# Kernel optimization log

Measured on AMD Instinct MI355X. Metric: run time of the kernel, lower is better.

Reference implementation:

```python
import jax, jax.numpy as jnp
import numpy as np

CODEBOOK_SIZE = 8192
EMBED_DIM = 256


def setup_inputs() -> dict:
    key = jax.random.key(0)
    k1, k2 = jax.random.split(key)
    z = jax.random.normal(k1, (8, 4096, EMBED_DIM), dtype=jnp.float32)
    # matches torch init: uniform_(-1/codebook_size, 1/codebook_size)
    codebook = jax.random.uniform(
        k2, (CODEBOOK_SIZE, EMBED_DIM), dtype=jnp.float32,
        minval=-1.0 / CODEBOOK_SIZE, maxval=1.0 / CODEBOOK_SIZE)
    return {"z": z, "codebook": codebook}


def reference(z, codebook):
    # z: [B, S, D]; codebook: [K, D]
    z_flat = z.reshape(-1, z.shape[-1])                      # [N, D]
    # ||z||^2 - 2 z.E^T + ||E||^2  -> [N, K]
    distances = (
        jnp.sum(z_flat * z_flat, axis=1, keepdims=True)
        - 2.0 * jnp.einsum("nd,kd->nk", z_flat, codebook)
        + jnp.sum(codebook * codebook, axis=1)
    )
    encoding_indices = jnp.argmin(distances, axis=1)         # [N]
    z_q = codebook[encoding_indices].reshape(z.shape)        # [B, S, D]
    return z_q, encoding_indices
```

## Files before the change

### kernel.cpp

```cpp
#include <hip/hip_runtime.h>


#define NROWS 32768
#define DIM   256
#define KCB   8192
#define CANDCAP 128
#define MARGIN  4.5e-4f
#define WBUF    320
#define NTILE   512

#define OFF_CAND  0
#define OFF_CNT   2097152
#define OFF_ZSQ   2129920
#define OFF_CSQ   2162688
#define OFF_CSQ1  2170880
#define OFF_OVL   2179072
#define OFF_OVC   2211840
#define OFF_IMG   2211856
#define OFF_IDX   8388608

using bf16x8 = __attribute__((ext_vector_type(8))) short;
using f32x4  = __attribute__((ext_vector_type(4))) float;

__device__ __forceinline__ unsigned short bf16rne(float f) {
    unsigned u = __float_as_uint(f);
    unsigned r = u + 0x7FFFu + ((u >> 16) & 1u);
    return (unsigned short)(r >> 16);
}

__device__ float np_sumsq_256(const float* __restrict__ p) {
#pragma clang fp contract(off)
    float blk[2];
    #pragma unroll
    for (int b = 0; b < 2; ++b) {
        const float* q = p + b * 128;
        float r[8];
        #pragma unroll
        for (int j = 0; j < 8; ++j) r[j] = __fmul_rn(q[j], q[j]);
        for (int i = 8; i < 128; i += 8) {
            #pragma unroll
            for (int j = 0; j < 8; ++j)
                r[j] = __fadd_rn(r[j], __fmul_rn(q[i + j], q[i + j]));
        }
        blk[b] = __fadd_rn(
            __fadd_rn(__fadd_rn(r[0], r[1]), __fadd_rn(r[2], r[3])),
            __fadd_rn(__fadd_rn(r[4], r[5]), __fadd_rn(r[6], r[7])));
    }
    return __fadd_rn(blk[0], blk[1]);
}

__global__ void vq_sumsq2_kernel(const float* __restrict__ z,
                                 const float* __restrict__ cb,
                                 float* __restrict__ zsq, float* __restrict__ csq) {
    int r = blockIdx.x * 256 + threadIdx.x;
    if (r < NROWS) zsq[r] = np_sumsq_256(z + (size_t)r * DIM);
    else if (r < NROWS + KCB) csq[r - NROWS] = np_sumsq_256(cb + (size_t)(r - NROWS) * DIM);
}

__global__ void vq_prepB_kernel(const float* __restrict__ cb,
                                const float* __restrict__ csq,
                                char* __restrict__ img, float* __restrict__ csq1,
                                unsigned* __restrict__ cnt, unsigned* __restrict__ ovc) {
    int t = blockIdx.x * 256 + threadIdx.x;
    if (t < NROWS) cnt[t] = 0;
    if (t == 0) *ovc = 0;
    if (t < 262144) {
        int s = t & 63, kk = (t >> 6) & 7, T = t >> 9;
        int code = s & 15, lhi = s >> 4;
        const float* src = cb + (size_t)(T * 16 + code) * DIM + kk * 32 + lhi * 8;
        float4 v0 = *reinterpret_cast<const float4*>(src);
        float4 v1 = *reinterpret_cast<const float4*>(src + 4);
        uint4 o;
        o.x = (unsigned)bf16rne(v0.x) | ((unsigned)bf16rne(v0.y) << 16);
        o.y = (unsigned)bf16rne(v0.z) | ((unsigned)bf16rne(v0.w) << 16);
        o.z = (unsigned)bf16rne(v1.x) | ((unsigned)bf16rne(v1.y) << 16);
        o.w = (unsigned)bf16rne(v1.z) | ((unsigned)bf16rne(v1.w) << 16);
        *reinterpret_cast<uint4*>(img + (size_t)T * 8192 + kk * 1024 + s * 16) = o;
    } else if (t < 262144 + KCB) {
        csq1[t - 262144] = csq[t - 262144] + 1.0f;
    }
}

__global__ __launch_bounds__(512, 2) void vq_screen_kernel(
    const float* __restrict__ z, const char* __restrict__ img,
    const float* __restrict__ csq1,
    unsigned* __restrict__ cnt, unsigned short* __restrict__ cand) {
    __shared__ unsigned runmin[128];
    __shared__ unsigned wcnt[8];
    __shared__ unsigned wbuf[8][WBUF];
    const int tid = threadIdx.x, lane = tid & 63, wid = tid >> 6;
    const int wr = wid >> 2, wc = wid & 3;
    const int l15 = lane & 15, lhi = lane >> 4;
    const int row0 = blockIdx.x * 128;
    const int tbase = wc * 128;

    bf16x8 ah[4][8];
    #pragma unroll
    for (int m = 0; m < 4; ++m) {
        const float* zr = z + (size_t)(row0 + wr * 64 + m * 16 + l15) * DIM;
        #pragma unroll
        for (int kk = 0; kk < 8; ++kk) {
            float4 v0 = *reinterpret_cast<const float4*>(zr + kk * 32 + lhi * 8);
            float4 v1 = *reinterpret_cast<const float4*>(zr + kk * 32 + lhi * 8 + 4);
            uint4 o;
            o.x = (unsigned)bf16rne(v0.x) | ((unsigned)bf16rne(v0.y) << 16);
            o.y = (unsigned)bf16rne(v0.z) | ((unsigned)bf16rne(v0.w) << 16);
            o.z = (unsigned)bf16rne(v1.x) | ((unsigned)bf16rne(v1.y) << 16);
            o.w = (unsigned)bf16rne(v1.z) | ((unsigned)bf16rne(v1.w) << 16);
            ah[m][kk] = __builtin_bit_cast(bf16x8, o);
        }
    }

    if (tid < 128) runmin[tid] = 0x7F800000u;
    if (tid < 8) wcnt[tid] = 0;
    __syncthreads();

    f32x4 acc[4];
    #pragma unroll
    for (int m = 0; m < 4; ++m) acc[m] = (f32x4){0.f, 0.f, 0.f, 0.f};

    const char*  gp = img + (size_t)tbase * 8192 + (size_t)lane * 16;
    const float* cp = csq1 + tbase * 16 + l15;
    int codeb = tbase * 16 + l15;

    uint4 bA[8]; float csA;
    uint4 bB[8]; float csB;

    auto PUSH = [&](int lr, int code) {
        unsigned pi = atomicAdd(&wcnt[wid], 1u);
        if (pi < WBUF) wbuf[wid][pi] = ((unsigned)lr << 13) | (unsigned)code;
        else {
            int grow = row0 + lr;
            unsigned gs = atomicAdd(&cnt[grow], 1u);
            if (gs < CANDCAP) cand[(size_t)grow * CANDCAP + gs] = (unsigned short)code;
        }
    };

#define LOADR(bh, cs)                                                     \
    {                                                                     \
        _Pragma("unroll")                                                 \
        for (int kk = 0; kk < 8; ++kk)                                    \
            bh[kk] = *reinterpret_cast<const uint4*>(gp + kk * 1024);     \
        cs = *cp;                                                         \
        gp += 8192; cp += 16;                                             \
    }

#define MFMAS(bh)                                                         \
    {                                                                     \
        __builtin_amdgcn_s_setprio(1);                                    \
        _Pragma("unroll")                                                 \
        for (int kk = 0; kk < 8; ++kk) {                                  \
            bf16x8 bhv = __builtin_bit_cast(bf16x8, bh[kk]);              \
            _Pragma("unroll")                                             \
            for (int m = 0; m < 4; ++m)                                   \
                acc[m] = __builtin_amdgcn_mfma_f32_16x16x32_bf16(         \
                    ah[m][kk], bhv, acc[m], 0, 0, 0);                     \
        }                                                                 \
        __builtin_amdgcn_s_setprio(0);                                    \
    }

#define EPI(csv)                                                          \
    {                                                                     \
        _Pragma("unroll")                                                 \
        for (int m = 0; m < 4; ++m) {                                     \
            const int lr0 = wr * 64 + m * 16 + lhi * 4;                   \
            uint4 rmb = *reinterpret_cast<const uint4*>(&runmin[lr0]);    \
            float s0 = fmaf(acc[m][0], -2.0f, csv);                       \
            float s1 = fmaf(acc[m][1], -2.0f, csv);                       \
            float s2 = fmaf(acc[m][2], -2.0f, csv);                       \
            float s3 = fmaf(acc[m][3], -2.0f, csv);                       \
            bool c0 = s0 < __uint_as_float(rmb.x) + MARGIN;               \
            bool c1 = s1 < __uint_as_float(rmb.y) + MARGIN;               \
            bool c2 = s2 < __uint_as_float(rmb.z) + MARGIN;               \
            bool c3 = s3 < __uint_as_float(rmb.w) + MARGIN;               \
            if (__any(c0 | c1 | c2 | c3)) {                               \
                if (c0) { if (s0 < __uint_as_float(rmb.x)) atomicMin(&runmin[lr0 + 0], __float_as_uint(s0)); PUSH(lr0 + 0, codeb); } \
                if (c1) { if (s1 < __uint_as_float(rmb.y)) atomicMin(&runmin[lr0 + 1], __float_as_uint(s1)); PUSH(lr0 + 1, codeb); } \
                if (c2) { if (s2 < __uint_as_float(rmb.z)) atomicMin(&runmin[lr0 + 2], __float_as_uint(s2)); PUSH(lr0 + 2, codeb); } \
                if (c3) { if (s3 < __uint_as_float(rmb.w)) atomicMin(&runmin[lr0 + 3], __float_as_uint(s3)); PUSH(lr0 + 3, codeb); } \
            }                                                             \
            acc[m] = (f32x4){0.f, 0.f, 0.f, 0.f};                         \
        }                                                                 \
        codeb += 16;                                                      \
    }

    LOADR(bA, csA);
    LOADR(bB, csB);
    MFMAS(bA);
    {
        #pragma unroll
        for (int m = 0; m < 4; ++m) {
            const int lr0 = wr * 64 + m * 16 + lhi * 4;
            #pragma unroll
            for (int r = 0; r < 4; ++r) {
                float s2 = fmaf(acc[m][r], -2.0f, csA);
                float sm = s2;
                sm = fminf(sm, __shfl_xor(sm, 1));
                sm = fminf(sm, __shfl_xor(sm, 2));
                sm = fminf(sm, __shfl_xor(sm, 4));
                sm = fminf(sm, __shfl_xor(sm, 8));
                if (l15 == 0) atomicMin(&runmin[lr0 + r], __float_as_uint(sm));
                if (s2 < sm + MARGIN) PUSH(lr0 + r, codeb);
            }
            acc[m] = (f32x4){0.f, 0.f, 0.f, 0.f};
        }
        codeb += 16;
    }
    LOADR(bA, csA);
    MFMAS(bB);
    EPI(csB);

    for (int ct = 2; ct < 128; ct += 2) {
        LOADR(bB, csB);
        MFMAS(bA);
        EPI(csA);
        LOADR(bA, csA);
        MFMAS(bB);
        EPI(csB);
    }

    unsigned n = wcnt[wid]; if (n > WBUF) n = WBUF;
    for (unsigned e = lane; e < n; e += 64) {
        unsigned u = wbuf[wid][e];
        int row = row0 + (int)(u >> 13);
        int code = (int)(u & 8191u);
        unsigned slot = atomicAdd(&cnt[row], 1u);
        if (slot < CANDCAP) cand[(size_t)row * CANDCAP + slot] = (unsigned short)code;
    }
#undef LOADR
#undef MFMAS
#undef EPI
}

__global__ __launch_bounds__(256) void vq_exact_kernel(
    const float* __restrict__ z, const float* __restrict__ cb,
    const float* __restrict__ zsq, const float* __restrict__ csq,
    const unsigned* __restrict__ cnt, const unsigned short* __restrict__ cand,
    unsigned* __restrict__ ovl, unsigned* __restrict__ ovc,
    float* __restrict__ idxF) {
    __shared__ float zrow[4][DIM];
    const int wid = threadIdx.x >> 6, lane = threadIdx.x & 63;
    const int row = blockIdx.x * 4 + wid;

    float4 zv4 = *reinterpret_cast<const float4*>(&z[(size_t)row * DIM + lane * 4]);
    *reinterpret_cast<float4*>(&zrow[wid][lane * 4]) = zv4;
    __syncthreads();

    const unsigned c = cnt[row];
    if (c == 0 || c > CANDCAP) {
        if (lane == 0) { unsigned s = atomicAdd(ovc, 1u); ovl[s] = row; }
        return;
    }

    const float Zr = zsq[row];
    const float4* cb4 = reinterpret_cast<const float4*>(cb);
    float best = 3.4e38f;
    int   bi   = 0x7FFFFFFF;

    for (int j = lane; j < (int)c; j += 64) {
        int k = cand[(size_t)row * CANDCAP + j];
        float a = 0.0f;
        #pragma unroll 8
        for (int q = 0; q < 64; ++q) {
            float4 cv = cb4[(size_t)k * 64 + q];
            float4 zv = *reinterpret_cast<const float4*>(&zrow[wid][q * 4]);
            a = fmaf(zv.x, cv.x, a); a = fmaf(zv.y, cv.y, a);
            a = fmaf(zv.z, cv.z, a); a = fmaf(zv.w, cv.w, a);
        }
        float sv = __fadd_rn(__fsub_rn(Zr, __fmul_rn(2.0f, a)), csq[k]);
        if (sv < best || (sv == best && k < bi)) { best = sv; bi = k; }
    }
    #pragma unroll
    for (int mk = 32; mk >= 1; mk >>= 1) {
        float ov = __shfl_xor(best, mk);
        int   oi = __shfl_xor(bi, mk);
        if (ov < best || (ov == best && oi < bi)) { best = ov; bi = oi; }
    }
    if (lane == 0) idxF[row] = (float)bi;
}

__global__ __launch_bounds__(256) void vq_cleanup_kernel(
    const float* __restrict__ z, const float* __restrict__ cb,
    const float* __restrict__ zsq, const float* __restrict__ csq,
    const unsigned* __restrict__ ovl, const unsigned* __restrict__ ovc,
    float* __restrict__ idxF) {
    __shared__ float zrow[DIM];
    __shared__ float wv[4]; __shared__ int wi[4];
    const int lane = threadIdx.x & 63, wid = threadIdx.x >> 6;
    const unsigned count = *ovc;
    for (unsigned w = blockIdx.x; w < count; w += gridDim.x) {
        const int row = ovl[w];
        __syncthreads();
        *reinterpret_cast<float4*>(&zrow[threadIdx.x * 4 & (DIM - 1)]) =
            *reinterpret_cast<const float4*>(&z[(size_t)row * DIM + (threadIdx.x * 4 & (DIM - 1))]);
        __syncthreads();
        const float Zr = zsq[row];
        const float4* cb4 = reinterpret_cast<const float4*>(cb);
        float best = 3.4e38f; int bi = 0x7FFFFFFF;
        for (int k = threadIdx.x; k < KCB; k += 256) {
            float a = 0.0f;
            #pragma unroll 8
            for (int q = 0; q < 64; ++q) {
                float4 cv = cb4[(size_t)k * 64 + q];
                float4 zv = *reinterpret_cast<const float4*>(&zrow[q * 4]);
                a = fmaf(zv.x, cv.x, a); a = fmaf(zv.y, cv.y, a);
                a = fmaf(zv.z, cv.z, a); a = fmaf(zv.w, cv.w, a);
            }
            float sv = __fadd_rn(__fsub_rn(Zr, __fmul_rn(2.0f, a)), csq[k]);
            if (sv < best || (sv == best && k < bi)) { best = sv; bi = k; }
        }
        #pragma unroll
        for (int mk = 32; mk >= 1; mk >>= 1) {
            float ov = __shfl_xor(best, mk);
            int   oi = __shfl_xor(bi, mk);
            if (ov < best || (ov == best && oi < bi)) { best = ov; bi = oi; }
        }
        if (lane == 0) { wv[wid] = best; wi[wid] = bi; }
        __syncthreads();
        if (threadIdx.x == 0) {
            #pragma unroll
            for (int u = 1; u < 4; ++u)
                if (wv[u] < best || (wv[u] == best && wi[u] < bi)) { best = wv[u]; bi = wi[u]; }
            idxF[row] = (float)bi;
        }
    }
}

__global__ void vq_gather_kernel(const float* __restrict__ cb,
                                 const float* __restrict__ idxF,
                                 float4* __restrict__ out4) {
    int g = blockIdx.x * blockDim.x + threadIdx.x;
    const float4* cb4 = reinterpret_cast<const float4*>(cb);
    for (int i = g; i < NROWS * 64; i += gridDim.x * blockDim.x) {
        int row = i >> 6, q = i & 63;
        int idx = (int)idxF[row];
        out4[i] = cb4[(size_t)idx * 64 + q];
    }
}

extern "C" void kernel_launch(void* const* d_in, const int* in_sizes, int n_in,
                              void* d_out, int out_size, void* d_ws, size_t ws_size,
                              hipStream_t stream) {
    const float* z  = (const float*)d_in[0];
    const float* cb = (const float*)d_in[1];
    float* out = (float*)d_out;

    unsigned short* candp = (unsigned short*)(out + OFF_CAND);
    unsigned*       cntp  = (unsigned*)(out + OFF_CNT);
    float*          zsq   = out + OFF_ZSQ;
    float*          csq   = out + OFF_CSQ;
    float*          csq1  = out + OFF_CSQ1;
    unsigned*       ovl   = (unsigned*)(out + OFF_OVL);
    unsigned*       ovc   = (unsigned*)(out + OFF_OVC);
    char*           img   = (char*)(out + OFF_IMG);
    float*          idxF  = out + OFF_IDX;

    vq_sumsq2_kernel<<<(NROWS + KCB) / 256, 256, 0, stream>>>(z, cb, zsq, csq);
    vq_prepB_kernel<<<1057, 256, 0, stream>>>(cb, csq, img, csq1, cntp, ovc);
    vq_screen_kernel<<<NROWS / 128, 512, 0, stream>>>(z, img, csq1, cntp, candp);
    vq_exact_kernel<<<NROWS / 4, 256, 0, stream>>>(z, cb, zsq, csq, cntp, candp, ovl, ovc, idxF);
    vq_cleanup_kernel<<<64, 256, 0, stream>>>(z, cb, zsq, csq, ovl, ovc, idxF);
    vq_gather_kernel<<<2048, 256, 0, stream>>>(cb, idxF, (float4*)out);
}
```

Before: 299.0 us.

## Merge prep kernels, fuse gather into exact/cleanup using workspace scratch

Folds the sum-of-squares kernel into the codebook bf16 packing kernel so one launch computes both norms and the image. When the workspace is large enough, scratch buffers move from the output to the workspace, so the exact and cleanup kernels can write the gathered codebook rows directly and the separate gather kernel is skipped. Also drops the MFMA priority hints in the screen kernel. This removes two launches and one pass over the indices, but adds a workspace-size dependency and an extra sync in cleanup.

Result: faster. 288.2 us (-3.6%).

```diff
diff --git a/kernel.cpp b/kernel.cpp
--- a/kernel.cpp
+++ b/kernel.cpp
@@ -7,17 +7,16 @@
 #define CANDCAP 128
 #define MARGIN  4.5e-4f
 #define WBUF    320
-#define NTILE   512
-
-#define OFF_CAND  0
-#define OFF_CNT   2097152
-#define OFF_ZSQ   2129920
-#define OFF_CSQ   2162688
-#define OFF_CSQ1  2170880
-#define OFF_OVL   2179072
-#define OFF_OVC   2211840
-#define OFF_IMG   2211856
-#define OFF_IDX   8388608
+
+#define SB_CAND  0u
+#define SB_CNT   8388608u
+#define SB_ZSQ   8519680u
+#define SB_CSQ   8650752u
+#define SB_CSQ1  8683520u
+#define SB_OVL   8716288u
+#define SB_OVC   8847360u
+#define SB_IMG   8847424u
+#define SB_NEED  13049920u
 
 using bf16x8 = __attribute__((ext_vector_type(8))) short;
 using f32x4  = __attribute__((ext_vector_type(4))) float;
@@ -49,18 +48,12 @@
     return __fadd_rn(blk[0], blk[1]);
 }
 
-__global__ void vq_sumsq2_kernel(const float* __restrict__ z,
-                                 const float* __restrict__ cb,
-                                 float* __restrict__ zsq, float* __restrict__ csq) {
-    int r = blockIdx.x * 256 + threadIdx.x;
-    if (r < NROWS) zsq[r] = np_sumsq_256(z + (size_t)r * DIM);
-    else if (r < NROWS + KCB) csq[r - NROWS] = np_sumsq_256(cb + (size_t)(r - NROWS) * DIM);
-}
-
-__global__ void vq_prepB_kernel(const float* __restrict__ cb,
-                                const float* __restrict__ csq,
-                                char* __restrict__ img, float* __restrict__ csq1,
-                                unsigned* __restrict__ cnt, unsigned* __restrict__ ovc) {
+__global__ void vq_prep_kernel(const float* __restrict__ z,
+                               const float* __restrict__ cb,
+                               char* __restrict__ img,
+                               float* __restrict__ zsq, float* __restrict__ csq,
+                               float* __restrict__ csq1,
+                               unsigned* __restrict__ cnt, unsigned* __restrict__ ovc) {
     int t = blockIdx.x * 256 + threadIdx.x;
     if (t < NROWS) cnt[t] = 0;
     if (t == 0) *ovc = 0;
@@ -77,7 +70,13 @@
         o.w = (unsigned)bf16rne(v1.z) | ((unsigned)bf16rne(v1.w) << 16);
         *reinterpret_cast<uint4*>(img + (size_t)T * 8192 + kk * 1024 + s * 16) = o;
     } else if (t < 262144 + KCB) {
-        csq1[t - 262144] = csq[t - 262144] + 1.0f;
+        int k = t - 262144;
+        float s = np_sumsq_256(cb + (size_t)k * DIM);
+        csq[k] = s;
+        csq1[k] = s + 1.0f;
+    } else if (t < 262144 + KCB + NROWS) {
+        int r = t - 262144 - KCB;
+        zsq[r] = np_sumsq_256(z + (size_t)r * DIM);
     }
 }
 
@@ -147,7 +146,6 @@
 
 #define MFMAS(bh)                                                         \
     {                                                                     \
-        __builtin_amdgcn_s_setprio(1);                                    \
         _Pragma("unroll")                                                 \
         for (int kk = 0; kk < 8; ++kk) {                                  \
             bf16x8 bhv = __builtin_bit_cast(bf16x8, bh[kk]);              \
@@ -156,7 +154,6 @@
                 acc[m] = __builtin_amdgcn_mfma_f32_16x16x32_bf16(         \
                     ah[m][kk], bhv, acc[m], 0, 0, 0);                     \
         }                                                                 \
-        __builtin_amdgcn_s_setprio(0);                                    \
     }
 
 #define EPI(csv)                                                          \
@@ -237,7 +234,7 @@
     const float* __restrict__ zsq, const float* __restrict__ csq,
     const unsigned* __restrict__ cnt, const unsigned short* __restrict__ cand,
     unsigned* __restrict__ ovl, unsigned* __restrict__ ovc,
-    float* __restrict__ idxF) {
+    float* __restrict__ idxF, float4* __restrict__ outz, int fused) {
     __shared__ float zrow[4][DIM];
     const int wid = threadIdx.x >> 6, lane = threadIdx.x & 63;
     const int row = blockIdx.x * 4 + wid;
@@ -277,15 +274,17 @@
         if (ov < best || (ov == best && oi < bi)) { best = ov; bi = oi; }
     }
     if (lane == 0) idxF[row] = (float)bi;
+    if (fused) outz[(size_t)row * 64 + lane] = cb4[(size_t)bi * 64 + lane];
 }
 
 __global__ __launch_bounds__(256) void vq_cleanup_kernel(
     const float* __restrict__ z, const float* __restrict__ cb,
     const float* __restrict__ zsq, const float* __restrict__ csq,
     const unsigned* __restrict__ ovl, const unsigned* __restrict__ ovc,
-    float* __restrict__ idxF) {
+    float* __restrict__ idxF, float4* __restrict__ outz, int fused) {
     __shared__ float zrow[DIM];
     __shared__ float wv[4]; __shared__ int wi[4];
+    __shared__ int sbi;
     const int lane = threadIdx.x & 63, wid = threadIdx.x >> 6;
     const unsigned count = *ovc;
     for (unsigned w = blockIdx.x; w < count; w += gridDim.x) {
@@ -321,8 +320,12 @@
             #pragma unroll
             for (int u = 1; u < 4; ++u)
                 if (wv[u] < best || (wv[u] == best && wi[u] < bi)) { best = wv[u]; bi = wi[u]; }
-            idxF[row] = (float)bi;
-        }
+            idxF[row] = (float)best >= 0 ? (float)bi : (float)bi;
+            sbi = bi;
+        }
+        __syncthreads();
+        if (fused && threadIdx.x < 64)
+            outz[(size_t)row * 64 + threadIdx.x] = cb4[(size_t)sbi * 64 + threadIdx.x];
     }
 }
 
@@ -345,20 +348,26 @@
     const float* cb = (const float*)d_in[1];
     float* out = (float*)d_out;
 
-    unsigned short* candp = (unsigned short*)(out + OFF_CAND);
-    unsigned*       cntp  = (unsigned*)(out + OFF_CNT);
-    float*          zsq   = out + OFF_ZSQ;
-    float*          csq   = out + OFF_CSQ;
-    float*          csq1  = out + OFF_CSQ1;
-    unsigned*       ovl   = (unsigned*)(out + OFF_OVL);
-    unsigned*       ovc   = (unsigned*)(out + OFF_OVC);
-    char*           img   = (char*)(out + OFF_IMG);
-    float*          idxF  = out + OFF_IDX;
-
-    vq_sumsq2_kernel<<<(NROWS + KCB) / 256, 256, 0, stream>>>(z, cb, zsq, csq);
-    vq_prepB_kernel<<<1057, 256, 0, stream>>>(cb, csq, img, csq1, cntp, ovc);
+    const int fused = (ws_size >= (size_t)SB_NEED) ? 1 : 0;
+    char* SB = fused ? (char*)d_ws : (char*)d_out;
+
+    unsigned short* candp = (unsigned short*)(SB + SB_CAND);
+    unsigned*       cntp  = (unsigned*)(SB + SB_CNT);
+    float*          zsq   = (float*)(SB + SB_ZSQ);
+    float*          csq   = (float*)(SB + SB_CSQ);
+    float*          csq1  = (float*)(SB + SB_CSQ1);
+    unsigned*       ovl   = (unsigned*)(SB + SB_OVL);
+    unsigned*       ovc   = (unsigned*)(SB + SB_OVC);
+    char*           img   = SB + SB_IMG;
+    float*          idxF  = out + 8388608;
+
+    vq_prep_kernel<<<(262144 + KCB + NROWS + 255) / 256, 256, 0, stream>>>(
+        z, cb, img, zsq, csq, csq1, cntp, ovc);
     vq_screen_kernel<<<NROWS / 128, 512, 0, stream>>>(z, img, csq1, cntp, candp);
-    vq_exact_kernel<<<NROWS / 4, 256, 0, stream>>>(z, cb, zsq, csq, cntp, candp, ovl, ovc, idxF);
-    vq_cleanup_kernel<<<64, 256, 0, stream>>>(z, cb, zsq, csq, ovl, ovc, idxF);
-    vq_gather_kernel<<<2048, 256, 0, stream>>>(cb, idxF, (float4*)out);
-}
+    vq_exact_kernel<<<NROWS / 4, 256, 0, stream>>>(
+        z, cb, zsq, csq, cntp, candp, ovl, ovc, idxF, (float4*)out, fused);
+    vq_cleanup_kernel<<<64, 256, 0, stream>>>(
+        z, cb, zsq, csq, ovl, ovc, idxF, (float4*)out, fused);
+    if (!fused)
+        vq_gather_kernel<<<2048, 256, 0, stream>>>(cb, idxF, (float4*)out);
+}
```
